# Kernel tuning notes

Hardware: AMD Instinct MI355X
Metric: run time of the kernel (lower is better)

Reference implementation:

```python
import jax, jax.numpy as jnp
import numpy as np

IN_F = 4096
OUT_F = 11008

def setup_inputs() -> dict:
    key = jax.random.key(0)
    k1, k2, k3, k4 = jax.random.split(key, 4)
    x = jax.random.normal(k1, (4, 128, IN_F), dtype=jnp.float32)
    # int8-style quantized weights stored as int32 in [-127, 127]
    quantized_weight = jax.random.randint(k2, (OUT_F, IN_F), -127, 128, dtype=jnp.int32)
    # per-output-row scale, kept away from zero
    scale = jax.random.uniform(k3, (OUT_F, 1), dtype=jnp.float32, minval=0.5, maxval=1.5)
    bias = jax.random.normal(k4, (OUT_F,), dtype=jnp.float32)
    return {"x": x, "quantized_weight": quantized_weight, "scale": scale, "bias": bias}

def reference(x, quantized_weight, scale, bias):
    # int8 dequantization: weight = q.float() / scale  -> [OUT_F, IN_F] fp32
    weight = quantized_weight.astype(jnp.float32) / scale
    # F.linear(x, weight, bias) == x @ weight.T + bias
    out = jnp.einsum('bsi,oi->bso', x, weight) + bias
    return out
```

## Files before the change

### kernel.cpp

```cpp
#include <hip/hip_runtime.h>
#include <hip/hip_bf16.h>
#include <stdint.h>

#define IN_F  4096
#define OUT_F 11008
#define MTOT  512

#define BM 128
#define BN 64
#define BK 64
#define NKT (IN_F / BK)
#define A_TILE_B (BM * BK * 2)
#define B_TILE_B (BN * BK * 2)
#define X_WS_BYTES ((size_t)MTOT * IN_F * 2)

typedef __attribute__((ext_vector_type(4))) float  f32x4;
typedef __attribute__((ext_vector_type(4))) int    i32x4;
typedef __attribute__((ext_vector_type(2))) unsigned u32x2;
typedef __attribute__((ext_vector_type(4))) unsigned u32x4;
typedef __attribute__((ext_vector_type(8))) __bf16 bf16x8;

__device__ __forceinline__ unsigned pack2bf16_rnd(float lo, float hi) {
    unsigned ulo = __builtin_bit_cast(unsigned, lo) + 0x8000u;
    unsigned uhi = __builtin_bit_cast(unsigned, hi) + 0x8000u;
    return __builtin_amdgcn_perm(uhi, ulo, 0x07060302u);
}
__device__ __forceinline__ unsigned pack2bf16_exact(float lo, float hi) {
    return __builtin_amdgcn_perm(__builtin_bit_cast(unsigned, hi),
                                 __builtin_bit_cast(unsigned, lo), 0x07060302u);
}

__device__ __forceinline__ void gload_lds16(const void* g, void* l) {
    __builtin_amdgcn_global_load_lds(
        (const __attribute__((address_space(1))) unsigned*)g,
        (__attribute__((address_space(3))) unsigned*)l, 16, 0, 0);
}

__global__ __launch_bounds__(256)
void xconv_kernel(const float* __restrict__ X, char* __restrict__ xws) {
    const int gid  = blockIdx.x * 256 + threadIdx.x;
    const int row  = gid >> 9;
    const int col0 = (gid & 511) * 8;
    const float* src = X + (size_t)row * IN_F + col0;
    f32x4 v0 = *(const f32x4*)(src);
    f32x4 v1 = *(const f32x4*)(src + 4);
    u32x4 o;
    o.x = pack2bf16_rnd(v0.x, v0.y);
    o.y = pack2bf16_rnd(v0.z, v0.w);
    o.z = pack2bf16_rnd(v1.x, v1.y);
    o.w = pack2bf16_rnd(v1.z, v1.w);
    const int mtile = row >> 7, row_l = row & 127;
    const int kt = col0 >> 6,  k_l  = col0 & 63;
    const int a = row_l * 128 + k_l * 2;
    const int p = a ^ ((row_l & 7) << 4);
    *(u32x4*)(xws + (size_t)mtile * (NKT * A_TILE_B)
                  + (size_t)kt * A_TILE_B + p) = o;
}

template<bool USE_WS>
__global__ __launch_bounds__(128, 2)
void qgemm_kernel(const float* __restrict__ X, const char* __restrict__ xws,
                  const int*   __restrict__ W,
                  const float* __restrict__ scale,
                  const float* __restrict__ bias,
                  float* __restrict__ Out)
{
    __shared__ __align__(16) char smem[2 * A_TILE_B + B_TILE_B];
    char* bufA0 = smem;
    char* bufA1 = smem + A_TILE_B;
    char* bufB  = smem + 2 * A_TILE_B;

    const int tid  = (int)threadIdx.x;
    const int lane = tid & 63;
    const int w    = tid >> 6;

    const int bid  = (int)blockIdx.x;
    const int lbid = (bid & 7) * 86 + (bid >> 3);
    const int mtile = lbid & 3;
    const int ntile = lbid >> 2;
    const int brow = mtile * BM;
    const int bcol = ntile * BN;

    const int srow  = tid >> 4;
    const int scol4 = tid & 15;
    const int* Wp = W + (size_t)(bcol + srow) * IN_F + scol4 * 4;
    const float* Xp = X + (size_t)(brow + srow) * IN_F + scol4 * 4;

    const char* xsrc = xws + (size_t)mtile * (NKT * A_TILE_B)
                     + w * 8192 + lane * 16;

    i32x4 rb[8];
    f32x4 acc[4][4];
    #pragma unroll
    for (int i = 0; i < 4; ++i)
        #pragma unroll
        for (int j = 0; j < 4; ++j)
            acc[i][j] = (f32x4){0.f, 0.f, 0.f, 0.f};

    #pragma unroll
    for (int k = 0; k < 8; ++k)
        rb[k] = *(const i32x4*)(Wp + (size_t)(k * 8) * IN_F);
    if constexpr (USE_WS) {
        #pragma unroll
        for (int c = 0; c < 8; ++c)
            gload_lds16(xsrc + c * 1024, bufA0 + w * 8192 + c * 1024);
    }

    for (int kt = 0; kt < NKT; ++kt) {
        char* curA = USE_WS ? ((kt & 1) ? bufA1 : bufA0) : bufA0;

        #pragma unroll
        for (int k = 0; k < 8; ++k) {
            const int row = srow + k * 8;
            const int off = (row * 128 + scol4 * 8) ^ ((row & 7) << 4);
            u32x2 bv;
            bv.x = pack2bf16_exact((float)rb[k].x, (float)rb[k].y);
            bv.y = pack2bf16_exact((float)rb[k].z, (float)rb[k].w);
            *(u32x2*)(bufB + off) = bv;
        }
        if constexpr (!USE_WS) {
            #pragma unroll
            for (int k = 0; k < 16; ++k) {
                f32x4 ra = *(const f32x4*)(Xp + (size_t)kt * BK
                                              + (size_t)(k * 8) * IN_F);
                const int row = srow + k * 8;
                const int off = (row * 128 + scol4 * 8) ^ ((row & 7) << 4);
                u32x2 av;
                av.x = pack2bf16_rnd(ra.x, ra.y);
                av.y = pack2bf16_rnd(ra.z, ra.w);
                *(u32x2*)(bufA0 + off) = av;
            }
        }
        __syncthreads();

        if (kt + 1 < NKT) {
            if constexpr (USE_WS) {
                char* nxtA = (kt & 1) ? bufA0 : bufA1;
                const char* xs = xsrc + (size_t)(kt + 1) * A_TILE_B;
                #pragma unroll
                for (int c = 0; c < 8; ++c)
                    gload_lds16(xs + c * 1024, nxtA + w * 8192 + c * 1024);
            }
            const int* Wk = Wp + (size_t)(kt + 1) * BK;
            #pragma unroll
            for (int k = 0; k < 8; ++k)
                rb[k] = *(const i32x4*)(Wk + (size_t)(k * 8) * IN_F);
        }

        #pragma unroll
        for (int ks = 0; ks < 2; ++ks) {
            bf16x8 af[4], bfr[4];
            #pragma unroll
            for (int mi = 0; mi < 4; ++mi) {
                const int row = w * 64 + mi * 16 + (lane & 15);
                const int off = (row * 128 + ks * 64 + (lane >> 4) * 16)
                                ^ ((row & 7) << 4);
                af[mi] = *(const bf16x8*)(curA + off);
            }
            #pragma unroll
            for (int ni = 0; ni < 4; ++ni) {
                const int row = ni * 16 + (lane & 15);
                const int off = (row * 128 + ks * 64 + (lane >> 4) * 16)
                                ^ ((row & 7) << 4);
                bfr[ni] = *(const bf16x8*)(bufB + off);
            }
            #pragma unroll
            for (int mi = 0; mi < 4; ++mi)
                #pragma unroll
                for (int ni = 0; ni < 4; ++ni)
                    acc[mi][ni] = __builtin_amdgcn_mfma_f32_16x16x32_bf16(
                        af[mi], bfr[ni], acc[mi][ni], 0, 0, 0);
        }
        __syncthreads();
    }

    #pragma unroll
    for (int ni = 0; ni < 4; ++ni) {
        const int col = bcol + ni * 16 + (lane & 15);
        const float inv = 1.0f / scale[col];
        const float bs  = bias[col];
        #pragma unroll
        for (int mi = 0; mi < 4; ++mi) {
            const int row0 = brow + w * 64 + mi * 16 + ((lane >> 4) << 2);
            #pragma unroll
            for (int j = 0; j < 4; ++j) {
                Out[(size_t)(row0 + j) * OUT_F + col] = acc[mi][ni][j] * inv + bs;
            }
        }
    }
}

extern "C" void kernel_launch(void* const* d_in, const int* in_sizes, int n_in,
                              void* d_out, int out_size, void* d_ws, size_t ws_size,
                              hipStream_t stream) {
    const float* X     = (const float*)d_in[0];
    const int*   W     = (const int*)d_in[1];
    const float* scale = (const float*)d_in[2];
    const float* bias  = (const float*)d_in[3];
    float* Out = (float*)d_out;

    const int grid = (MTOT / BM) * (OUT_F / BN);

    if (ws_size >= X_WS_BYTES) {
        char* xws = (char*)d_ws;
        xconv_kernel<<<(MTOT * IN_F / 8) / 256, 256, 0, stream>>>(X, xws);
        qgemm_kernel<true><<<grid, 128, 0, stream>>>(X, xws, W, scale, bias, Out);
    } else {
        qgemm_kernel<false><<<grid, 128, 0, stream>>>(X, nullptr, W, scale, bias, Out);
    }
}
```

Before: 92.00 us.

## Split K dimension in two with atomic accumulation into zeroed output

```diff
diff --git a/kernel.cpp b/kernel.cpp
--- a/kernel.cpp
+++ b/kernel.cpp
@@ -9,7 +9,9 @@
 #define BM 128
 #define BN 64
 #define BK 64
-#define NKT (IN_F / BK)
+#define NKT   (IN_F / BK)
+#define KSPL  2
+#define NKT_S (NKT / KSPL)
 #define A_TILE_B (BM * BK * 2)
 #define B_TILE_B (BN * BK * 2)
 #define X_WS_BYTES ((size_t)MTOT * IN_F * 2)
@@ -57,13 +59,12 @@
                   + (size_t)kt * A_TILE_B + p) = o;
 }
 
-template<bool USE_WS>
 __global__ __launch_bounds__(128, 2)
-void qgemm_kernel(const float* __restrict__ X, const char* __restrict__ xws,
-                  const int*   __restrict__ W,
-                  const float* __restrict__ scale,
-                  const float* __restrict__ bias,
-                  float* __restrict__ Out)
+void qgemm_split_kernel(const char* __restrict__ xws,
+                        const int*   __restrict__ W,
+                        const float* __restrict__ scale,
+                        const float* __restrict__ bias,
+                        float* __restrict__ Out)
 {
     __shared__ __align__(16) char smem[2 * A_TILE_B + B_TILE_B];
     char* bufA0 = smem;
@@ -75,19 +76,20 @@
     const int w    = tid >> 6;
 
     const int bid  = (int)blockIdx.x;
-    const int lbid = (bid & 7) * 86 + (bid >> 3);
-    const int mtile = lbid & 3;
-    const int ntile = lbid >> 2;
+    const int lbid = (bid & 7) * 172 + (bid >> 3);
+    const int kspl  = lbid & 1;
+    const int mtile = (lbid >> 1) & 3;
+    const int ntile = lbid >> 3;
     const int brow = mtile * BM;
     const int bcol = ntile * BN;
+    const int kt0  = kspl * NKT_S;
 
     const int srow  = tid >> 4;
     const int scol4 = tid & 15;
-    const int* Wp = W + (size_t)(bcol + srow) * IN_F + scol4 * 4;
-    const float* Xp = X + (size_t)(brow + srow) * IN_F + scol4 * 4;
+    const int* Wp = W + (size_t)(bcol + srow) * IN_F + (size_t)kt0 * BK + scol4 * 4;
 
     const char* xsrc = xws + (size_t)mtile * (NKT * A_TILE_B)
-                     + w * 8192 + lane * 16;
+                     + (size_t)kt0 * A_TILE_B + w * 8192 + lane * 16;
 
     i32x4 rb[8];
     f32x4 acc[4][4];
@@ -100,14 +102,12 @@
     #pragma unroll
     for (int k = 0; k < 8; ++k)
         rb[k] = *(const i32x4*)(Wp + (size_t)(k * 8) * IN_F);
-    if constexpr (USE_WS) {
-        #pragma unroll
-        for (int c = 0; c < 8; ++c)
-            gload_lds16(xsrc + c * 1024, bufA0 + w * 8192 + c * 1024);
-    }
-
-    for (int kt = 0; kt < NKT; ++kt) {
-        char* curA = USE_WS ? ((kt & 1) ? bufA1 : bufA0) : bufA0;
+    #pragma unroll
+    for (int c = 0; c < 8; ++c)
+        gload_lds16(xsrc + c * 1024, bufA0 + w * 8192 + c * 1024);
+
+    for (int kt = 0; kt < NKT_S; ++kt) {
+        char* curA = (kt & 1) ? bufA1 : bufA0;
 
         #pragma unroll
         for (int k = 0; k < 8; ++k) {
@@ -118,29 +118,14 @@
             bv.y = pack2bf16_exact((float)rb[k].z, (float)rb[k].w);
             *(u32x2*)(bufB + off) = bv;
         }
-        if constexpr (!USE_WS) {
-            #pragma unroll
-            for (int k = 0; k < 16; ++k) {
-                f32x4 ra = *(const f32x4*)(Xp + (size_t)kt * BK
-                                              + (size_t)(k * 8) * IN_F);
-                const int row = srow + k * 8;
-                const int off = (row * 128 + scol4 * 8) ^ ((row & 7) << 4);
-                u32x2 av;
-                av.x = pack2bf16_rnd(ra.x, ra.y);
-                av.y = pack2bf16_rnd(ra.z, ra.w);
-                *(u32x2*)(bufA0 + off) = av;
-            }
-        }
-        __syncthreads();
-
-        if (kt + 1 < NKT) {
-            if constexpr (USE_WS) {
-                char* nxtA = (kt & 1) ? bufA0 : bufA1;
-                const char* xs = xsrc + (size_t)(kt + 1) * A_TILE_B;
-                #pragma unroll
-                for (int c = 0; c < 8; ++c)
-                    gload_lds16(xs + c * 1024, nxtA + w * 8192 + c * 1024);
-            }
+        __syncthreads();
+
+        if (kt + 1 < NKT_S) {
+            char* nxtA = (kt & 1) ? bufA0 : bufA1;
+            const char* xs = xsrc + (size_t)(kt + 1) * A_TILE_B;
+            #pragma unroll
+            for (int c = 0; c < 8; ++c)
+                gload_lds16(xs + c * 1024, nxtA + w * 8192 + c * 1024);
             const int* Wk = Wp + (size_t)(kt + 1) * BK;
             #pragma unroll
             for (int k = 0; k < 8; ++k)
@@ -178,14 +163,113 @@
     for (int ni = 0; ni < 4; ++ni) {
         const int col = bcol + ni * 16 + (lane & 15);
         const float inv = 1.0f / scale[col];
-        const float bs  = bias[col];
+        const float bs  = (kspl == 0) ? bias[col] : 0.0f;
         #pragma unroll
         for (int mi = 0; mi < 4; ++mi) {
             const int row0 = brow + w * 64 + mi * 16 + ((lane >> 4) << 2);
             #pragma unroll
             for (int j = 0; j < 4; ++j) {
+                atomicAdd(&Out[(size_t)(row0 + j) * OUT_F + col],
+                          acc[mi][ni][j] * inv + bs);
+            }
+        }
+    }
+}
+
+__global__ __launch_bounds__(128, 2)
+void qgemm_fallback_kernel(const float* __restrict__ X,
+                           const int*   __restrict__ W,
+                           const float* __restrict__ scale,
+                           const float* __restrict__ bias,
+                           float* __restrict__ Out)
+{
+    __shared__ __align__(16) char smem[A_TILE_B + B_TILE_B];
+    char* bufA = smem;
+    char* bufB = smem + A_TILE_B;
+
+    const int tid  = (int)threadIdx.x;
+    const int lane = tid & 63;
+    const int w    = tid >> 6;
+
+    const int bid  = (int)blockIdx.x;
+    const int lbid = (bid & 7) * 86 + (bid >> 3);
+    const int mtile = lbid & 3;
+    const int ntile = lbid >> 2;
+    const int brow = mtile * BM;
+    const int bcol = ntile * BN;
+
+    const int srow  = tid >> 4;
+    const int scol4 = tid & 15;
+    const int* Wp = W + (size_t)(bcol + srow) * IN_F + scol4 * 4;
+    const float* Xp = X + (size_t)(brow + srow) * IN_F + scol4 * 4;
+
+    f32x4 acc[4][4];
+    #pragma unroll
+    for (int i = 0; i < 4; ++i)
+        #pragma unroll
+        for (int j = 0; j < 4; ++j)
+            acc[i][j] = (f32x4){0.f, 0.f, 0.f, 0.f};
+
+    for (int kt = 0; kt < NKT; ++kt) {
+        #pragma unroll
+        for (int k = 0; k < 8; ++k) {
+            i32x4 rb = *(const i32x4*)(Wp + (size_t)kt * BK + (size_t)(k * 8) * IN_F);
+            const int row = srow + k * 8;
+            const int off = (row * 128 + scol4 * 8) ^ ((row & 7) << 4);
+            u32x2 bv;
+            bv.x = pack2bf16_exact((float)rb.x, (float)rb.y);
+            bv.y = pack2bf16_exact((float)rb.z, (float)rb.w);
+            *(u32x2*)(bufB + off) = bv;
+        }
+        #pragma unroll
+        for (int k = 0; k < 16; ++k) {
+            f32x4 ra = *(const f32x4*)(Xp + (size_t)kt * BK + (size_t)(k * 8) * IN_F);
+            const int row = srow + k * 8;
+            const int off = (row * 128 + scol4 * 8) ^ ((row & 7) << 4);
+            u32x2 av;
+            av.x = pack2bf16_rnd(ra.x, ra.y);
+            av.y = pack2bf16_rnd(ra.z, ra.w);
+            *(u32x2*)(bufA + off) = av;
+        }
+        __syncthreads();
+        #pragma unroll
+        for (int ks = 0; ks < 2; ++ks) {
+            bf16x8 af[4], bfr[4];
+            #pragma unroll
+            for (int mi = 0; mi < 4; ++mi) {
+                const int row = w * 64 + mi * 16 + (lane & 15);
+                const int off = (row * 128 + ks * 64 + (lane >> 4) * 16)
+                                ^ ((row & 7) << 4);
+                af[mi] = *(const bf16x8*)(bufA + off);
+            }
+            #pragma unroll
+            for (int ni = 0; ni < 4; ++ni) {
+                const int row = ni * 16 + (lane & 15);
+                const int off = (row * 128 + ks * 64 + (lane >> 4) * 16)
+                                ^ ((row & 7) << 4);
+                bfr[ni] = *(const bf16x8*)(bufB + off);
+            }
+            #pragma unroll
+            for (int mi = 0; mi < 4; ++mi)
+                #pragma unroll
+                for (int ni = 0; ni < 4; ++ni)
+                    acc[mi][ni] = __builtin_amdgcn_mfma_f32_16x16x32_bf16(
+                        af[mi], bfr[ni], acc[mi][ni], 0, 0, 0);
+        }
+        __syncthreads();
+    }
+
+    #pragma unroll
+    for (int ni = 0; ni < 4; ++ni) {
+        const int col = bcol + ni * 16 + (lane & 15);
+        const float inv = 1.0f / scale[col];
+        const float bs  = bias[col];
+        #pragma unroll
+        for (int mi = 0; mi < 4; ++mi) {
+            const int row0 = brow + w * 64 + mi * 16 + ((lane >> 4) << 2);
+            #pragma unroll
+            for (int j = 0; j < 4; ++j)
                 Out[(size_t)(row0 + j) * OUT_F + col] = acc[mi][ni][j] * inv + bs;
-            }
         }
     }
 }
@@ -199,13 +283,14 @@
     const float* bias  = (const float*)d_in[3];
     float* Out = (float*)d_out;
 
-    const int grid = (MTOT / BM) * (OUT_F / BN);
-
     if (ws_size >= X_WS_BYTES) {
         char* xws = (char*)d_ws;
+        hipMemsetAsync(Out, 0, (size_t)out_size * sizeof(float), stream);
         xconv_kernel<<<(MTOT * IN_F / 8) / 256, 256, 0, stream>>>(X, xws);
-        qgemm_kernel<true><<<grid, 128, 0, stream>>>(X, xws, W, scale, bias, Out);
+        const int grid = (MTOT / BM) * (OUT_F / BN) * KSPL;
+        qgemm_split_kernel<<<grid, 128, 0, stream>>>(xws, W, scale, bias, Out);
     } else {
-        qgemm_kernel<false><<<grid, 128, 0, stream>>>(X, nullptr, W, scale, bias, Out);
-    }
-}
+        const int grid = (MTOT / BM) * (OUT_F / BN);
+        qgemm_fallback_kernel<<<grid, 128, 0, stream>>>(X, W, scale, bias, Out);
+    }
+}
```

Measured after the change: 118.0 us. +28.3%, slower.
